# Performance work log

Measured on AMD Instinct MI355X. Metric: run time of the kernel, lower is better.

The kernel has to match this reference:

```python
import jax, jax.numpy as jnp
import numpy as np

C_S, C_HID, H, P, V = 128, 16, 12, 4, 8
EPS = 1e-08
SOFTPLUS_INV_1 = 0.541324854612918


def _pts_from_linear(x, n_pts):
    # torch: split [..., 3*n] into 3 chunks of n, stack on dim=-1 -> [..., n, 3]
    B, N = x.shape[:2]
    return jnp.moveaxis(x.reshape(B, N, 3, n_pts), -2, -1)


def setup_inputs() -> dict:
    key = jax.random.key(0)
    ks = jax.random.split(key, 16)
    B, N = 2, 512
    hc = H * C_HID            # 192
    hpq = H * P * 3           # 144
    hpkv = H * (P + V) * 3    # 432
    cat_dim = H * (C_HID + V * 4)  # 576
    sc = 0.02
    inp = {
        "s": jax.random.normal(ks[0], (B, N, C_S), jnp.float32),
        "R": jax.random.normal(ks[1], (B, N, 3, 3), jnp.float32),
        "t": jax.random.normal(ks[2], (B, N, 3), jnp.float32),
        "pair_mask": jnp.ones((B, N, N), jnp.float32),
        "Wq": jax.random.normal(ks[3], (C_S, hc), jnp.float32) * sc,
        "bq": jnp.zeros((hc,), jnp.float32),
        "Wkv": jax.random.normal(ks[4], (C_S, 2 * hc), jnp.float32) * sc,
        "bkv": jnp.zeros((2 * hc,), jnp.float32),
        "Wqp": jax.random.normal(ks[5], (C_S, hpq), jnp.float32) * sc,
        "bqp": jnp.zeros((hpq,), jnp.float32),
        "Wkvp": jax.random.normal(ks[6], (C_S, hpkv), jnp.float32) * sc,
        "bkvp": jnp.zeros((hpkv,), jnp.float32),
        "head_weights": jnp.full((H,), SOFTPLUS_INV_1, jnp.float32),
        "Wout": jax.random.normal(ks[7], (cat_dim, C_S), jnp.float32) * sc,
        "bout": jnp.zeros((C_S,), jnp.float32),
    }
    return inp


def reference(s, R, t, pair_mask, Wq, bq, Wkv, bkv, Wqp, bqp, Wkvp, bkvp,
              head_weights, Wout, bout):
    B, N, _ = s.shape
    # scalar q/k/v
    q = (s @ Wq + bq).reshape(B, N, H, C_HID)
    kv = (s @ Wkv + bkv).reshape(B, N, H, 2 * C_HID)
    k, v = kv[..., :C_HID], kv[..., C_HID:]

    # point q/k/v in global frame: R x + t
    qp = _pts_from_linear(s @ Wqp + bqp, H * P)           # [B,N,HP,3]
    qp = jnp.einsum('bnij,bnpj->bnpi', R, qp) + t[:, :, None]
    qp = qp.reshape(B, N, H, P, 3)
    kvp = _pts_from_linear(s @ Wkvp + bkvp, H * (P + V))  # [B,N,H(P+V),3]
    kvp = jnp.einsum('bnij,bnpj->bnpi', R, kvp) + t[:, :, None]
    kvp = kvp.reshape(B, N, H, P + V, 3)
    kp, vp = kvp[..., :P, :], kvp[..., P:, :]

    # scalar attention logits [B,H,N,N]
    a = jnp.einsum('bihc,bjhc->bhij', q, k) * (1.0 / np.sqrt(3 * C_HID))

    # point-distance bias: sum_p ||q_i - k_j||^2 via |q|^2+|k|^2-2q.k
    sq_q = jnp.sum(qp * qp, axis=(-1, -2))   # [B,N,H]
    sq_k = jnp.sum(kp * kp, axis=(-1, -2))   # [B,N,H]
    cross = jnp.einsum('bihpc,bjhpc->bhij', qp, kp)
    d2 = (jnp.swapaxes(sq_q, 1, 2)[..., :, None]
          + jnp.swapaxes(sq_k, 1, 2)[..., None, :]
          - 2.0 * cross)                      # [B,H,N,N]
    hw = jax.nn.softplus(head_weights) * np.sqrt(1.0 / (3 * (P * 9.0 / 2)))
    pt_att = d2 * hw[None, :, None, None] * (-0.5)

    square_mask = 100000.0 * (pair_mask - 1.0)            # [B,N,N]
    a = jax.nn.softmax(a + pt_att + square_mask[:, None], axis=-1)

    # scalar output
    o = jnp.einsum('bhij,bjhc->bihc', a, v).reshape(B, N, H * C_HID)

    # point output, rotated back to local frame: R^T (x - t) form -> R^T x - t
    o_pt = jnp.einsum('bhij,bjhvc->bihvc', a, vp)         # [B,N,H,V,3]
    o_pt = jnp.einsum('bnji,bnhvj->bnhvi', R, o_pt) - t[:, :, None, None]
    o_pt_norm = jnp.sqrt(jnp.sum(o_pt * o_pt, axis=-1) + EPS).reshape(B, N, H * V)
    o_pt_flat = o_pt.reshape(B, N, H * V, 3)

    cat = jnp.concatenate(
        [o, o_pt_flat[..., 0], o_pt_flat[..., 1], o_pt_flat[..., 2], o_pt_norm],
        axis=-1)                                           # [B,N,576]
    return cat @ Wout + bout
```

## Files before the change

kernel.cpp:

```cpp
#include <hip/hip_runtime.h>
#include <hip/hip_bf16.h>
#include <math.h>

#define H_    12
#define B_    2
#define N_    512
#define BH_   (B_*H_)
#define QSCALE 0.14433756729740643f
#define CPT_K  0.13608276348795434f

#define OFF_WPP  1245184
#define OFF_WOP  1318912
#define OFF_BIA  1355776
#define OFF_QB   1356928
#define OFF_KP   1553536
#define OFF_VP   1750144
#define OFF_SA   2045056
#define OFF_SB   2057344
#define OFF_CATP 2069632

typedef __attribute__((ext_vector_type(8))) short sh8;
typedef __attribute__((ext_vector_type(4))) float f32x4;
typedef unsigned short u16t;

static __device__ __forceinline__ u16t f2b(float x) {
    __hip_bfloat16 h = __float2bfloat16(x);
    return *reinterpret_cast<u16t*>(&h);
}
static __device__ __forceinline__ int catp_idx(int tok, int col) {
    return (tok >> 4)*9216 + (col >> 5)*512 + ((col >> 3) & 3)*128
         + (tok & 15)*8 + (col & 7);
}

__global__ __launch_bounds__(256) void convert_kernel(
    const float* __restrict__ Wq,  const float* __restrict__ bq,
    const float* __restrict__ Wkv, const float* __restrict__ bkv,
    const float* __restrict__ Wqp, const float* __restrict__ bqp,
    const float* __restrict__ Wkvp,const float* __restrict__ bkvp,
    const float* __restrict__ Wout, float* __restrict__ ws)
{
    const int g = blockIdx.x * 256 + threadIdx.x;
    union { sh8 v; u16t u[8]; } pk;

    if (g < 18432) {
        int u = g;
        int n = u & 63, kq = (u >> 6) & 3, ks = (u >> 8) & 3, nt = u >> 10;
        int col = nt*64 + n, k0 = ks*32 + kq*8;
        const float* w; int lc, od;
        if (col < 192)      { w = Wq;   lc = col;     od = 192; }
        else if (col < 576) { w = Wkv;  lc = col-192; od = 384; }
        else if (col < 720) { w = Wqp;  lc = col-576; od = 144; }
        else                { w = Wkvp; lc = col-720; od = 432; }
        #pragma unroll
        for (int j = 0; j < 8; ++j) pk.u[j] = f2b(w[(k0+j)*od + lc]);
        *((sh8*)((u16t*)(ws + OFF_WPP)) + u) = pk.v;
    } else if (g < 27648) {
        int u = g - 18432;
        int n = u & 63, kq = (u >> 6) & 3, rem = u >> 8;
        int ks = rem % 18, nt = rem / 18;
        int col = nt*64 + n, k0 = ks*32 + kq*8;
        #pragma unroll
        for (int j = 0; j < 8; ++j) pk.u[j] = f2b(Wout[(k0+j)*128 + col]);
        *((sh8*)((u16t*)(ws + OFF_WOP)) + u) = pk.v;
    } else if (g < 28800) {
        int col = g - 27648;
        float bv;
        if (col < 192)      bv = bq[col];
        else if (col < 576) bv = bkv[col-192];
        else if (col < 720) bv = bqp[col-576];
        else                bv = bkvp[col-720];
        ws[OFF_BIA + col] = bv;
    }
}

__global__ __launch_bounds__(512) void projpack_kernel(
    const float* __restrict__ s,
    const float* __restrict__ Rg, const float* __restrict__ tg,
    const float* __restrict__ hwg, float* __restrict__ ws)
{
    __shared__ float ldsP[8][1160];

    u16t* Qb = (u16t*)(ws + OFF_QB);
    u16t* Kp = (u16t*)(ws + OFF_KP);
    u16t* Vp = (u16t*)(ws + OFF_VP);
    float* sa_g = ws + OFF_SA;
    float* sb_g = ws + OFF_SB;

    const int tid  = threadIdx.x;
    const int w    = tid >> 6, lane = tid & 63;
    const int kq   = lane >> 4, lx = lane & 15;
    const int tok0 = blockIdx.x * 8;
    const int b    = tok0 >> 9, n0 = tok0 & 511;

    sh8 afr[4];
    #pragma unroll
    for (int ks = 0; ks < 4; ++ks) {
        const float* src = s + (tok0 + (lx & 7))*128 + ks*32 + kq*8;
        float4 u0 = *(const float4*)(src);
        float4 u1 = *(const float4*)(src+4);
        union { sh8 v; u16t u[8]; } pk;
        pk.u[0]=f2b(u0.x); pk.u[1]=f2b(u0.y); pk.u[2]=f2b(u0.z); pk.u[3]=f2b(u0.w);
        pk.u[4]=f2b(u1.x); pk.u[5]=f2b(u1.y); pk.u[6]=f2b(u1.z); pk.u[7]=f2b(u1.w);
        afr[ks] = pk.v;
    }

    const sh8* Bp = (const sh8*)((const u16t*)(ws + OFF_WPP));
    const float* bias = ws + OFF_BIA;

    #pragma unroll 3
    for (int g = 0; g < 9; ++g) {
        int gg = w*9 + g;
        int nt = gg >> 2, nq = gg & 3;
        f32x4 acc = {0.f,0.f,0.f,0.f};
        #pragma unroll
        for (int ks = 0; ks < 4; ++ks) {
            sh8 bf = Bp[((nt*4 + ks)*4 + kq)*64 + nq*16 + lx];
            acc = __builtin_amdgcn_mfma_f32_16x16x32_bf16(afr[ks], bf, acc, 0, 0, 0);
        }
        float bv = bias[gg*16 + lx];
        if (kq < 2) {
            #pragma unroll
            for (int r = 0; r < 4; ++r)
                ldsP[kq*4 + r][gg*16 + lx] = acc[r] + bv;
        }
    }
    __syncthreads();

    for (int idx = tid; idx < 8*48; idx += 512) {
        int tk = idx / 48, p = idx % 48;
        int tok = tok0 + tk;
        const float* Rr = Rg + tok*9;
        const float* tr = tg + tok*3;
        float x0 = ldsP[tk][576 +  0 + p];
        float x1 = ldsP[tk][576 + 48 + p];
        float x2 = ldsP[tk][576 + 96 + p];
        ldsP[tk][576 +  0 + p] = Rr[0]*x0 + Rr[1]*x1 + Rr[2]*x2 + tr[0];
        ldsP[tk][576 + 48 + p] = Rr[3]*x0 + Rr[4]*x1 + Rr[5]*x2 + tr[1];
        ldsP[tk][576 + 96 + p] = Rr[6]*x0 + Rr[7]*x1 + Rr[8]*x2 + tr[2];
    }
    for (int idx = tid; idx < 8*144; idx += 512) {
        int tk = idx / 144, p = idx % 144;
        int tok = tok0 + tk;
        const float* Rr = Rg + tok*9;
        const float* tr = tg + tok*3;
        float x0 = ldsP[tk][720 +   0 + p];
        float x1 = ldsP[tk][720 + 144 + p];
        float x2 = ldsP[tk][720 + 288 + p];
        ldsP[tk][720 +   0 + p] = Rr[0]*x0 + Rr[1]*x1 + Rr[2]*x2 + tr[0];
        ldsP[tk][720 + 144 + p] = Rr[3]*x0 + Rr[4]*x1 + Rr[5]*x2 + tr[1];
        ldsP[tk][720 + 288 + p] = Rr[6]*x0 + Rr[7]*x1 + Rr[8]*x2 + tr[2];
    }
    __syncthreads();

    for (int idx = tid; idx < 8*24; idx += 512) {
        int tk = idx / 24, r2 = idx % 24, h = r2 >> 1, half = r2 & 1;
        float hx = hwg[h];
        float sp = (hx > 20.f) ? hx : log1pf(__expf(hx));
        float c_pt = -0.5f * sp * CPT_K;
        union { sh8 v[2]; u16t u[16]; } pk;
        if (half == 0) {
            #pragma unroll
            for (int e = 0; e < 16; ++e) pk.u[e] = f2b(ldsP[tk][h*16 + e] * QSCALE);
        } else {
            float qs = -2.f * c_pt;
            #pragma unroll
            for (int e = 0; e < 12; ++e)
                pk.u[e] = f2b(ldsP[tk][576 + (e%3)*48 + h*4 + e/3] * qs);
            pk.u[12]=0; pk.u[13]=0; pk.u[14]=0; pk.u[15]=0;
        }
        u16t* dst = Qb + ((b*H_+h)*N_ + n0 + tk)*32 + half*16;
        *(sh8*)dst = pk.v[0];
        *(sh8*)(dst+8) = pk.v[1];
    }
    for (int idx = tid; idx < 8*48; idx += 512) {
        int tk = idx / 48, r2 = idx % 48, h = r2 >> 2, fq = r2 & 3;
        int j = n0 + tk, bh = b*H_ + h;
        union { sh8 v; u16t u[8]; } pk;
        #pragma unroll
        for (int e = 0; e < 8; ++e) {
            int c = fq*8 + e;
            float val;
            if (c < 16)      val = ldsP[tk][192 + h*32 + c];
            else if (c < 28) val = ldsP[tk][720 + ((c-16)%3)*144 + h*12 + (c-16)/3];
            else             val = 0.f;
            pk.u[e] = f2b(val);
        }
        *(sh8*)(Kp + bh*16384 + (j>>4)*512 + fq*128 + (j&15)*8) = pk.v;
    }
    for (int idx = tid; idx < 480; idx += 512) {
        int h = idx / 40, d = idx % 40;
        int bh = b*H_ + h;
        union { sh8 v; u16t u[8]; } pk;
        #pragma unroll
        for (int e = 0; e < 8; ++e) {
            float val;
            if (d < 16) val = ldsP[e][192 + h*32 + 16 + d];
            else        val = ldsP[e][720 + ((d-16)%3)*144 + h*12 + 4 + (d-16)/3];
            pk.u[e] = f2b(val);
        }
        int j = n0;
        *(sh8*)(Vp + bh*24576 + (j>>5)*1536 + (d>>4)*512 + ((j>>3)&3)*128
                + (d&15)*8) = pk.v;
    }
    for (int idx = tid; idx < 8*12; idx += 512) {
        int tk = idx / 12, h = idx % 12;
        float hx = hwg[h];
        float sp = (hx > 20.f) ? hx : log1pf(__expf(hx));
        float c_pt = -0.5f * sp * CPT_K;
        float sq = 0.f, sk = 0.f;
        #pragma unroll
        for (int pp = 0; pp < 4; ++pp)
            #pragma unroll
            for (int c = 0; c < 3; ++c) {
                float a = ldsP[tk][576 + c*48  + h*4  + pp]; sq += a*a;
                float k = ldsP[tk][720 + c*144 + h*12 + pp]; sk += k*k;
            }
        sa_g[(b*H_+h)*N_ + n0 + tk] = c_pt * sq;
        sb_g[(b*H_+h)*N_ + n0 + tk] = c_pt * sk;
    }
}

__global__ __launch_bounds__(512, 2) void attn_kernel(
    const float* __restrict__ Rg, const float* __restrict__ tg,
    const float* __restrict__ maskg, float* __restrict__ ws)
{
    __shared__ u16t smP[8*16*72];
    __shared__ float mbuf[4*64*20];
    __shared__ float obuf[64*32];

    const u16t* Qb = (const u16t*)(ws + OFF_QB);
    const u16t* Kp = (const u16t*)(ws + OFF_KP);
    const u16t* Vp = (const u16t*)(ws + OFF_VP);
    const float* sa_g = ws + OFF_SA;
    const float* sb_g = ws + OFF_SB;
    u16t* catp = (u16t*)(ws + OFF_CATP);

    const int tid  = threadIdx.x;
    const int w    = tid >> 6, lane = tid & 63;
    const int rg   = w & 3, jh = w >> 2;
    const int kq   = lane >> 4, lx = lane & 15;
    const int bh   = blockIdx.x >> 3;
    const int it   = blockIdx.x & 7;
    const int b    = bh / H_, h = bh % H_;
    const int i0   = it * 64;

    sh8 qfrag = *(const sh8*)(Qb + (bh*N_ + i0 + rg*16 + lx)*32 + kq*8);
    float sa_r[4];
    #pragma unroll
    for (int r = 0; r < 4; ++r)
        sa_r[r] = sa_g[bh*N_ + i0 + rg*16 + kq*4 + r];

    float m_run[4] = {-1e30f,-1e30f,-1e30f,-1e30f};
    float l_run[4] = {0.f,0.f,0.f,0.f};
    f32x4 oc0 = {0.f,0.f,0.f,0.f}, oc1 = oc0, oc2 = oc0;

    const float* mrow = maskg + (size_t)(b*N_ + i0 + rg*16 + kq*4)*N_ + lx;
    u16t* pw = smP + w*1152;

    for (int t = 0; t < 4; ++t) {
        const int jt = jh*4 + t;
        const int j0 = jt * 64;

        f32x4 sc[4];
        #pragma unroll
        for (int st = 0; st < 4; ++st) {
            sh8 kf = *(const sh8*)(Kp + bh*16384 + (jt*4+st)*512 + kq*128 + lx*8);
            f32x4 z = {0.f,0.f,0.f,0.f};
            sc[st] = __builtin_amdgcn_mfma_f32_16x16x32_bf16(qfrag, kf, z, 0, 0, 0);
        }
        float sbv[4];
        #pragma unroll
        for (int st = 0; st < 4; ++st) sbv[st] = sb_g[bh*N_ + j0 + st*16 + lx];
        float mb[16];
        #pragma unroll
        for (int r = 0; r < 4; ++r)
            #pragma unroll
            for (int st = 0; st < 4; ++st)
                mb[r*4+st] = mrow[r*N_ + j0 + st*16];

        float L[16];
        #pragma unroll
        for (int st = 0; st < 4; ++st)
            #pragma unroll
            for (int r = 0; r < 4; ++r)
                L[st*4+r] = sc[st][r] + sa_r[r] + sbv[st] + 1e5f*(mb[r*4+st] - 1.f);

        #pragma unroll
        for (int r = 0; r < 4; ++r) {
            float tm = fmaxf(fmaxf(L[0*4+r], L[1*4+r]), fmaxf(L[2*4+r], L[3*4+r]));
            tm = fmaxf(tm, __shfl_xor(tm, 1));
            tm = fmaxf(tm, __shfl_xor(tm, 2));
            tm = fmaxf(tm, __shfl_xor(tm, 4));
            tm = fmaxf(tm, __shfl_xor(tm, 8));
            float mnew = fmaxf(m_run[r], tm);
            float al = __expf(m_run[r] - mnew);
            m_run[r] = mnew;
            l_run[r] *= al;
            oc0[r] *= al; oc1[r] *= al; oc2[r] *= al;
        }
        #pragma unroll
        for (int st = 0; st < 4; ++st)
            #pragma unroll
            for (int r = 0; r < 4; ++r) {
                float p = __expf(L[st*4+r] - m_run[r]);
                l_run[r] += p;
                pw[(kq*4+r)*72 + st*16 + lx] = f2b(p);
            }
        #pragma unroll
        for (int c = 0; c < 2; ++c) {
            sh8 pa = *(const sh8*)(pw + lx*72 + c*32 + kq*8);
            #pragma unroll
            for (int nq = 0; nq < 3; ++nq) {
                sh8 vf = *(const sh8*)(Vp + bh*24576 + (jt*2+c)*1536 + nq*512
                                        + kq*128 + lx*8);
                if (nq == 0) oc0 = __builtin_amdgcn_mfma_f32_16x16x32_bf16(pa, vf, oc0, 0,0,0);
                if (nq == 1) oc1 = __builtin_amdgcn_mfma_f32_16x16x32_bf16(pa, vf, oc1, 0,0,0);
                if (nq == 2) oc2 = __builtin_amdgcn_mfma_f32_16x16x32_bf16(pa, vf, oc2, 0,0,0);
            }
        }
    }

    if (jh == 1) {
        float* mb = mbuf + (rg*64 + lane)*20;
        #pragma unroll
        for (int r = 0; r < 4; ++r) {
            mb[r]      = m_run[r];
            mb[4 + r]  = l_run[r];
            mb[8 + r]  = oc0[r];
            mb[12 + r] = oc1[r];
            mb[16 + r] = oc2[r];
        }
    }
    __syncthreads();
    if (jh == 0) {
        const float* mb = mbuf + (rg*64 + lane)*20;
        float linv[4];
        #pragma unroll
        for (int r = 0; r < 4; ++r) {
            float mB = mb[r];
            float ms = fmaxf(m_run[r], mB);
            float eA = __expf(m_run[r] - ms);
            float eB = __expf(mB - ms);
            float l = l_run[r]*eA + mb[4+r]*eB;
            oc0[r] = oc0[r]*eA + mb[8+r]*eB;
            oc1[r] = oc1[r]*eA + mb[12+r]*eB;
            oc2[r] = oc2[r]*eA + mb[16+r]*eB;
            l += __shfl_xor(l, 1); l += __shfl_xor(l, 2);
            l += __shfl_xor(l, 4); l += __shfl_xor(l, 8);
            linv[r] = 1.f / l;
        }

        #pragma unroll
        for (int r = 0; r < 4; ++r) {
            int tok = b*N_ + i0 + rg*16 + kq*4 + r;
            catp[catp_idx(tok, h*16 + lx)] = f2b(oc0[r] * linv[r]);
            obuf[(rg*16 + kq*4 + r)*32 + lx]      = oc1[r] * linv[r];
            obuf[(rg*16 + kq*4 + r)*32 + 16 + lx] = oc2[r] * linv[r];
        }

        #pragma unroll
        for (int tsk = 0; tsk < 2; ++tsk) {
            int task = lane + tsk*64;
            int r = task >> 3, pv = task & 7;
            int tok = b*N_ + i0 + rg*16 + r;
            const float* Rr = Rg + tok*9;
            const float* tr = tg + tok*3;
            float g0 = obuf[(rg*16 + r)*32 + pv*3 + 0];
            float g1 = obuf[(rg*16 + r)*32 + pv*3 + 1];
            float g2 = obuf[(rg*16 + r)*32 + pv*3 + 2];
            float px = Rr[0]*g0 + Rr[3]*g1 + Rr[6]*g2 - tr[0];
            float py = Rr[1]*g0 + Rr[4]*g1 + Rr[7]*g2 - tr[1];
            float pz = Rr[2]*g0 + Rr[5]*g1 + Rr[8]*g2 - tr[2];
            float nrm = sqrtf(px*px + py*py + pz*pz + 1e-8f);
            catp[catp_idx(tok, 192 + h*8 + pv)] = f2b(px);
            catp[catp_idx(tok, 288 + h*8 + pv)] = f2b(py);
            catp[catp_idx(tok, 384 + h*8 + pv)] = f2b(pz);
            catp[catp_idx(tok, 480 + h*8 + pv)] = f2b(nrm);
        }
    }
}

__global__ __launch_bounds__(512) void out_kernel(
    const float* __restrict__ bout, const float* __restrict__ ws,
    float* __restrict__ out)
{
    __shared__ float part[4][64][4];

    const int tid = threadIdx.x;
    const int w = tid >> 6, lane = tid & 63;
    const int cg = w & 3, kh = w >> 2;
    const int lx = lane & 15, kq = lane >> 4;
    const int nt = blockIdx.x, mt = blockIdx.y;

    const sh8* Ap = (const sh8*)((const u16t*)(ws + OFF_CATP));
    const sh8* Bp = (const sh8*)((const u16t*)(ws + OFF_WOP));

    f32x4 acc = {0.f,0.f,0.f,0.f};
    #pragma unroll 3
    for (int i = 0; i < 9; ++i) {
        int ks = kh*9 + i;
        sh8 af = Ap[((mt*18 + ks)*4 + kq)*16 + lx];
        sh8 bf = Bp[((nt*18 + ks)*4 + kq)*64 + cg*16 + lx];
        acc = __builtin_amdgcn_mfma_f32_16x16x32_bf16(af, bf, acc, 0, 0, 0);
    }
    if (kh == 1) {
        #pragma unroll
        for (int r = 0; r < 4; ++r) part[cg][lane][r] = acc[r];
    }
    __syncthreads();
    if (kh == 0) {
        int col = nt*64 + cg*16 + lx;
        float bv = bout[col];
        #pragma unroll
        for (int r = 0; r < 4; ++r) {
            int row = mt*16 + kq*4 + r;
            out[row*128 + col] = acc[r] + part[cg][lane][r] + bv;
        }
    }
}

extern "C" void kernel_launch(void* const* d_in, const int* in_sizes, int n_in,
                              void* d_out, int out_size, void* d_ws, size_t ws_size,
                              hipStream_t stream) {
    const float* s    = (const float*)d_in[0];
    const float* R    = (const float*)d_in[1];
    const float* t    = (const float*)d_in[2];
    const float* mask = (const float*)d_in[3];
    const float* Wq   = (const float*)d_in[4];
    const float* bq   = (const float*)d_in[5];
    const float* Wkv  = (const float*)d_in[6];
    const float* bkv  = (const float*)d_in[7];
    const float* Wqp  = (const float*)d_in[8];
    const float* bqp  = (const float*)d_in[9];
    const float* Wkvp = (const float*)d_in[10];
    const float* bkvp = (const float*)d_in[11];
    const float* hw   = (const float*)d_in[12];
    const float* Wout = (const float*)d_in[13];
    const float* bout = (const float*)d_in[14];
    float* ws  = (float*)d_ws;
    float* out = (float*)d_out;

    convert_kernel<<<113, 256, 0, stream>>>(Wq, bq, Wkv, bkv,
                                            Wqp, bqp, Wkvp, bkvp, Wout, ws);
    projpack_kernel<<<128, 512, 0, stream>>>(s, R, t, hw, ws);
    attn_kernel<<<BH_*8, 512, 0, stream>>>(R, t, mask, ws);
    out_kernel<<<dim3(2, 64), 512, 0, stream>>>(bout, ws, out);
}
```

Measured before the change: 111.9 us.

## Split attention and output GEMM across more blocks with 4-way key/K splits

The attention kernel now gives each block 32 query rows instead of 64. Its 8 waves split into 2 row groups by 4 key quarters, and a 4-way online-softmax merge runs through shared memory, which doubles the grid to 384 blocks. The output GEMM uses 32-column tiles with a 4-way K split across waves, which doubles its grid as well. The goal is better occupancy and latency hiding on a GPU with many CUs. The cost is more reduction work, extra shared-memory traffic, and redundant Q loads per block.

```diff
diff --git a/kernel.cpp b/kernel.cpp
--- a/kernel.cpp
+++ b/kernel.cpp
@@ -225,8 +225,8 @@
     const float* __restrict__ maskg, float* __restrict__ ws)
 {
     __shared__ u16t smP[8*16*72];
-    __shared__ float mbuf[4*64*20];
-    __shared__ float obuf[64*32];
+    __shared__ float mbuf[3*128*20];
+    __shared__ float obuf[32*32];
 
     const u16t* Qb = (const u16t*)(ws + OFF_QB);
     const u16t* Kp = (const u16t*)(ws + OFF_KP);
@@ -237,12 +237,12 @@
 
     const int tid  = threadIdx.x;
     const int w    = tid >> 6, lane = tid & 63;
-    const int rg   = w & 3, jh = w >> 2;
+    const int rg   = w & 1, jh = w >> 1;
     const int kq   = lane >> 4, lx = lane & 15;
-    const int bh   = blockIdx.x >> 3;
-    const int it   = blockIdx.x & 7;
+    const int bh   = blockIdx.x >> 4;
+    const int it   = blockIdx.x & 15;
     const int b    = bh / H_, h = bh % H_;
-    const int i0   = it * 64;
+    const int i0   = it * 32;
 
     sh8 qfrag = *(const sh8*)(Qb + (bh*N_ + i0 + rg*16 + lx)*32 + kq*8);
     float sa_r[4];
@@ -257,8 +257,9 @@
     const float* mrow = maskg + (size_t)(b*N_ + i0 + rg*16 + kq*4)*N_ + lx;
     u16t* pw = smP + w*1152;
 
-    for (int t = 0; t < 4; ++t) {
-        const int jt = jh*4 + t;
+    #pragma unroll
+    for (int t = 0; t < 2; ++t) {
+        const int jt = jh*2 + t;
         const int j0 = jt * 64;
 
         f32x4 sc[4];
@@ -320,8 +321,8 @@
         }
     }
 
-    if (jh == 1) {
-        float* mb = mbuf + (rg*64 + lane)*20;
+    if (jh > 0) {
+        float* mb = mbuf + ((jh-1)*128 + rg*64 + lane)*20;
         #pragma unroll
         for (int r = 0; r < 4; ++r) {
             mb[r]      = m_run[r];
@@ -333,18 +334,25 @@
     }
     __syncthreads();
     if (jh == 0) {
-        const float* mb = mbuf + (rg*64 + lane)*20;
         float linv[4];
         #pragma unroll
         for (int r = 0; r < 4; ++r) {
-            float mB = mb[r];
-            float ms = fmaxf(m_run[r], mB);
+            float ms = m_run[r];
+            #pragma unroll
+            for (int q = 0; q < 3; ++q)
+                ms = fmaxf(ms, mbuf[(q*128 + rg*64 + lane)*20 + r]);
             float eA = __expf(m_run[r] - ms);
-            float eB = __expf(mB - ms);
-            float l = l_run[r]*eA + mb[4+r]*eB;
-            oc0[r] = oc0[r]*eA + mb[8+r]*eB;
-            oc1[r] = oc1[r]*eA + mb[12+r]*eB;
-            oc2[r] = oc2[r]*eA + mb[16+r]*eB;
+            float l = l_run[r]*eA;
+            oc0[r] *= eA; oc1[r] *= eA; oc2[r] *= eA;
+            #pragma unroll
+            for (int q = 0; q < 3; ++q) {
+                const float* mb = mbuf + (q*128 + rg*64 + lane)*20;
+                float e = __expf(mb[r] - ms);
+                l      += mb[4+r]*e;
+                oc0[r] += mb[8+r]*e;
+                oc1[r] += mb[12+r]*e;
+                oc2[r] += mb[16+r]*e;
+            }
             l += __shfl_xor(l, 1); l += __shfl_xor(l, 2);
             l += __shfl_xor(l, 4); l += __shfl_xor(l, 8);
             linv[r] = 1.f / l;
@@ -384,37 +392,40 @@
     const float* __restrict__ bout, const float* __restrict__ ws,
     float* __restrict__ out)
 {
-    __shared__ float part[4][64][4];
+    __shared__ float part[2][3][64][4];
 
     const int tid = threadIdx.x;
     const int w = tid >> 6, lane = tid & 63;
-    const int cg = w & 3, kh = w >> 2;
+    const int cg = w & 1, kh = w >> 1;
     const int lx = lane & 15, kq = lane >> 4;
     const int nt = blockIdx.x, mt = blockIdx.y;
 
     const sh8* Ap = (const sh8*)((const u16t*)(ws + OFF_CATP));
     const sh8* Bp = (const sh8*)((const u16t*)(ws + OFF_WOP));
 
+    const int ke0 = (kh*18) >> 2;
+    const int ke1 = ((kh+1)*18) >> 2;
+
     f32x4 acc = {0.f,0.f,0.f,0.f};
-    #pragma unroll 3
-    for (int i = 0; i < 9; ++i) {
-        int ks = kh*9 + i;
+    #pragma unroll 5
+    for (int ks = ke0; ks < ke1; ++ks) {
         sh8 af = Ap[((mt*18 + ks)*4 + kq)*16 + lx];
-        sh8 bf = Bp[((nt*18 + ks)*4 + kq)*64 + cg*16 + lx];
+        sh8 bf = Bp[(((nt>>1)*18 + ks)*4 + kq)*64 + (nt&1)*32 + cg*16 + lx];
         acc = __builtin_amdgcn_mfma_f32_16x16x32_bf16(af, bf, acc, 0, 0, 0);
     }
-    if (kh == 1) {
-        #pragma unroll
-        for (int r = 0; r < 4; ++r) part[cg][lane][r] = acc[r];
+    if (kh > 0) {
+        #pragma unroll
+        for (int r = 0; r < 4; ++r) part[cg][kh-1][lane][r] = acc[r];
     }
     __syncthreads();
     if (kh == 0) {
-        int col = nt*64 + cg*16 + lx;
+        int col = nt*32 + cg*16 + lx;
         float bv = bout[col];
         #pragma unroll
         for (int r = 0; r < 4; ++r) {
             int row = mt*16 + kq*4 + r;
-            out[row*128 + col] = acc[r] + part[cg][lane][r] + bv;
+            out[row*128 + col] = acc[r] + part[cg][0][lane][r]
+                               + part[cg][1][lane][r] + part[cg][2][lane][r] + bv;
         }
     }
 }
@@ -443,6 +454,6 @@
     convert_kernel<<<113, 256, 0, stream>>>(Wq, bq, Wkv, bkv,
                                             Wqp, bqp, Wkvp, bkvp, Wout, ws);
     projpack_kernel<<<128, 512, 0, stream>>>(s, R, t, hw, ws);
-    attn_kernel<<<BH_*8, 512, 0, stream>>>(R, t, mask, ws);
-    out_kernel<<<dim3(2, 64), 512, 0, stream>>>(bout, ws, out);
-}
+    attn_kernel<<<BH_*16, 512, 0, stream>>>(R, t, mask, ws);
+    out_kernel<<<dim3(4, 64), 512, 0, stream>>>(bout, ws, out);
+}
```

Measured after the change: 109.8 us. Within noise of the previous version (-1.9%).
